# Kernel tuning notes

Hardware: AMD Instinct MI355X
Metric: run time of the kernel (lower is better)

## Reference

```python
import jax, jax.numpy as jnp
import numpy as np
from jax import lax

DN = ('NCHW', 'OIHW', 'NCHW')

def conv2d(x, w, b):
    y = lax.conv_general_dilated(x, w, (1, 1), 'SAME', dimension_numbers=DN)
    return y + b[None, :, None, None]


def setup_inputs() -> dict:
    key = jax.random.key(0)
    ks = jax.random.split(key, 12)
    B, H, W = 16, 256, 256
    def wt(k, shape):
        return jax.random.normal(k, shape, jnp.float32) * 0.05
    return {
        'x': jax.random.normal(ks[0], (B, 1, H, W), jnp.float32),
        'g': jax.random.normal(ks[1], (B, 1, H, W), jnp.float32),
        # conv1 branch (x): 1->64 relu 64->1
        'w1a': wt(ks[2], (64, 1, 3, 3)), 'b1a': jnp.zeros((64,), jnp.float32),
        'w1b': wt(ks[3], (1, 64, 3, 3)), 'b1b': jnp.zeros((1,), jnp.float32),
        # conv2 branch (g): 1->64 relu 64->1
        'w2a': wt(ks[4], (64, 1, 3, 3)), 'b2a': jnp.zeros((64,), jnp.float32),
        'w2b': wt(ks[5], (1, 64, 3, 3)), 'b2b': jnp.zeros((1,), jnp.float32),
        # dynamic filter head: 2->64 relu 64->64 relu 64->81, softmax over taps
        'wfa': wt(ks[6], (64, 2, 3, 3)), 'bfa': jnp.zeros((64,), jnp.float32),
        'wfb': wt(ks[7], (64, 64, 3, 3)), 'bfb': jnp.zeros((64,), jnp.float32),
        'wfc': wt(ks[8], (81, 64, 3, 3)), 'bfc': jnp.zeros((81,), jnp.float32),
    }


def reference(x, g, w1a, b1a, w1b, b1b, w2a, b2a, w2b, b2b,
              wfa, bfa, wfb, bfb, wfc, bfc):
    # feature branches -> 1 channel each
    x_ = conv2d(jax.nn.relu(conv2d(x, w1a, b1a)), w1b, b1b)   # [B,1,H,W]
    g_ = conv2d(jax.nn.relu(conv2d(g, w2a, b2a)), w2b, b2b)   # [B,1,H,W]
    feat = jnp.concatenate([x_, g_], axis=1)                   # [B,2,H,W]
    # per-pixel 9x9 dynamic filter (81 taps), softmax-normalized
    h = jax.nn.relu(conv2d(feat, wfa, bfa))
    h = jax.nn.relu(conv2d(h, wfb, bfb))
    filt = jax.nn.softmax(conv2d(h, wfc, bfc), axis=1)         # [B,81,H,W]
    # unfold: 9x9 neighborhoods with zero pad 4, row-major tap order
    # matches torch unfold(2,9,1).unfold(3,9,1).permute(0,1,4,5,2,3)
    patches = lax.conv_general_dilated_patches(
        x, (9, 9), (1, 1), padding=((4, 4), (4, 4)),
        dimension_numbers=DN)                                  # [B,81,H,W]
    out = jnp.sum(patches * filt, axis=1, keepdims=True)       # [B,1,H,W]
    return out
```

## Files before the change

### kernel.cpp

```cpp
#include <hip/hip_runtime.h>

#define NB 16
#define HH 256
#define WW 256
#define NPIX (HH*WW)

typedef _Float16 f16;
typedef _Float16 f16x8 __attribute__((ext_vector_type(8)));
typedef float f32x4 __attribute__((ext_vector_type(4)));

__device__ __forceinline__ int swzoff(int p, int c) {
    return p * 64 + ((((c >> 3) ^ (p & 7)) << 3) | (c & 7));
}

__global__ __launch_bounds__(256) void prepack_kernel(
    const float* __restrict__ w1a, const float* __restrict__ w2a,
    const float* __restrict__ w1b, const float* __restrict__ w2b,
    const float* __restrict__ wfa, const float* __restrict__ wfb,
    const float* __restrict__ wfc,
    f16* __restrict__ pA1, f16* __restrict__ pA2, f16* __restrict__ pWa,
    f16* __restrict__ pBs1, f16* __restrict__ pBs2,
    f16* __restrict__ pWbF, f16* __restrict__ pWcF)
{
    int i = blockIdx.x * 256 + threadIdx.x;
    if (i < 2048) {
        int c = i >> 5, k = i & 31;
        pA1[i] = (f16)(k < 9 ? w1a[c * 9 + k] : 0.f);
        pA2[i] = (f16)(k < 9 ? w2a[c * 9 + k] : 0.f);
        pWa[i] = (f16)(k < 18 ? wfa[c * 18 + k] : 0.f);
    }
    if (i < 1024) {
        int r = i >> 6, cin = i & 63;
        pBs1[i] = (f16)(r < 9 ? w1b[cin * 9 + r] : 0.f);
        pBs2[i] = (f16)(r < 9 ? w2b[cin * 9 + r] : 0.f);
    }
    if (i < 36864) {
        int kk = i / 2048, r = i & 2047;
        int mt = r >> 9, e = r & 511;
        int l = e >> 3, j = e & 7;
        int cout = mt * 16 + (l & 15);
        int k = kk * 32 + ((l >> 4) << 3) + j;
        int tap = k >> 6, cin = k & 63;
        pWbF[i] = (f16)wfb[(cout * 64 + cin) * 9 + tap];
    }
    if (i < 55296) {
        int kk = i / 3072, r = i % 3072;
        int mt = r >> 9, e = r & 511;
        int l = e >> 3, j = e & 7;
        int cout = mt * 16 + (l & 15);
        int k = kk * 32 + ((l >> 4) << 3) + j;
        int tap = k >> 6, cin = k & 63;
        pWcF[i] = (f16)(cout < 81 ? wfc[(cout * 64 + cin) * 9 + tap] : 0.f);
    }
}

__global__ __launch_bounds__(256, 3) void k1_branch(
    const float* __restrict__ x, const float* __restrict__ g,
    const float* __restrict__ b1a, const float* __restrict__ b2a,
    const float* __restrict__ b1b, const float* __restrict__ b2b,
    const f16* __restrict__ pA1, const f16* __restrict__ pA2,
    const f16* __restrict__ pBs1, const f16* __restrict__ pBs2,
    float* __restrict__ feat)
{
    __shared__ f16 xt[400];
    __shared__ f16 hid[20736];
    __shared__ f16 part[9 * 328];
    __shared__ float bA[64];

    const int tid = threadIdx.x;
    const int wid = tid >> 6, lane = tid & 63;
    const int gq = lane >> 4, cl = lane & 15;
    const int x0 = blockIdx.x * 16, y0 = blockIdx.y * 16;
    const int b = blockIdx.z >> 1, br = blockIdx.z & 1;

    const float* in = (br ? g : x) + (size_t)b * NPIX;
    const f16* pA = br ? pA2 : pA1;
    const f16* pBs = br ? pBs2 : pBs1;
    const float bscal = (br ? b2b : b1b)[0];

    for (int t = tid; t < 400; t += 256) {
        int r = t / 20, c = t % 20;
        int gy = y0 - 2 + r, gx = x0 - 2 + c;
        xt[t] = (f16)(((unsigned)gy < (unsigned)HH && (unsigned)gx < (unsigned)WW)
                          ? in[gy * WW + gx] : 0.f);
    }
    if (tid < 64) bA[tid] = (br ? b2a : b1a)[tid];

    int koff[8];
    #pragma unroll
    for (int j = 0; j < 8; j++) {
        int k = gq * 8 + j;
        int kc = k < 9 ? k : 0;
        koff[j] = (kc / 3) * 20 + (kc % 3);
    }

    f16x8 afA[4];
    #pragma unroll
    for (int mt = 0; mt < 4; mt++)
        afA[mt] = *(const f16x8*)&pA[(mt * 16 + cl) * 32 + gq * 8];
    f16x8 afS0 = *(const f16x8*)&pBs[cl * 64 + gq * 8];
    f16x8 afS1 = *(const f16x8*)&pBs[cl * 64 + 32 + gq * 8];
    __syncthreads();

    #pragma unroll
    for (int it = 0; it < 6; it++) {
        int nt = wid + it * 4;
        if (nt < 21) {
            int p = nt * 16 + cl;
            int pc = p > 323 ? 323 : p;
            int py = pc / 18, px = pc - 18 * py;
            int base = py * 20 + px;
            f16x8 bf;
            #pragma unroll
            for (int j = 0; j < 8; j++) bf[j] = xt[base + koff[j]];
            int gy = y0 - 1 + py, gx = x0 - 1 + px;
            bool ok = (p < 324) &&
                      ((unsigned)gy < (unsigned)HH && (unsigned)gx < (unsigned)WW);
            #pragma unroll
            for (int mt = 0; mt < 4; mt++) {
                f32x4 z = {0.f, 0.f, 0.f, 0.f};
                f32x4 acc = __builtin_amdgcn_mfma_f32_16x16x32_f16(afA[mt], bf, z, 0, 0, 0);
                if (p < 324) {
                    int c0 = mt * 16 + gq * 4;
                    union { f16 h[4]; uint2 u2; } pk;
                    #pragma unroll
                    for (int r = 0; r < 4; r++)
                        pk.h[r] = (f16)(ok ? fmaxf(acc[r] + bA[c0 + r], 0.f) : 0.f);
                    *(uint2*)&hid[swzoff(p, c0)] = pk.u2;
                }
            }
        }
    }
    __syncthreads();

    #pragma unroll
    for (int it = 0; it < 6; it++) {
        int nt = wid + it * 4;
        if (nt < 21) {
            int p = nt * 16 + cl;
            int pc = p > 323 ? 323 : p;
            f16x8 bf0 = *(const f16x8*)&hid[swzoff(pc, gq * 8)];
            f16x8 bf1 = *(const f16x8*)&hid[swzoff(pc, 32 + gq * 8)];
            f32x4 z = {0.f, 0.f, 0.f, 0.f};
            f32x4 d = __builtin_amdgcn_mfma_f32_16x16x32_f16(afS0, bf0, z, 0, 0, 0);
            d = __builtin_amdgcn_mfma_f32_16x16x32_f16(afS1, bf1, d, 0, 0, 0);
            #pragma unroll
            for (int r = 0; r < 4; r++) {
                int tap = gq * 4 + r;
                if (tap < 9 && p < 324)
                    part[tap * 328 + p] = (f16)d[r];
            }
        }
    }
    __syncthreads();

    {
        int ty = tid >> 4, tx = tid & 15;
        float s = bscal;
        #pragma unroll
        for (int u = 0; u < 3; u++)
            #pragma unroll
            for (int v = 0; v < 3; v++)
                s += (float)part[(u * 3 + v) * 328 + (ty + u) * 18 + tx + v];
        feat[((size_t)(b * 2 + br)) * NPIX + (y0 + ty) * WW + x0 + tx] = s;
    }
}

__global__ __launch_bounds__(256, 3) void k2_wfab(
    const float* __restrict__ feat, const f16* __restrict__ pWa,
    const f16* __restrict__ pWbF, const float* __restrict__ bfa,
    const float* __restrict__ bfb, f16* __restrict__ h2g, int b0)
{
    __shared__ f16 ftt[800];
    __shared__ f16 hid[20736];
    __shared__ float bA[64];
    __shared__ float bB[64];

    const int tid = threadIdx.x;
    const int wid = tid >> 6, lane = tid & 63;
    const int gq = lane >> 4, cl = lane & 15;
    const int x0 = blockIdx.x * 16, y0 = blockIdx.y * 16;
    const int ci = blockIdx.z, b = b0 + ci;

    for (int t = tid; t < 800; t += 256) {
        int cin = t / 400, p = t - 400 * cin;
        int r = p / 20, c = p - 20 * r;
        int gy = y0 - 2 + r, gx = x0 - 2 + c;
        ftt[t] = (f16)(((unsigned)gy < (unsigned)HH && (unsigned)gx < (unsigned)WW)
                           ? feat[((size_t)(b * 2 + cin)) * NPIX + gy * WW + gx] : 0.f);
    }
    if (tid < 64) { bA[tid] = bfa[tid]; bB[tid] = bfb[tid]; }

    int koff[8];
    #pragma unroll
    for (int j = 0; j < 8; j++) {
        int k = gq * 8 + j;
        int kc = k < 18 ? k : 0;
        int cin = kc >= 9 ? 1 : 0;
        int tap = kc - 9 * cin;
        koff[j] = cin * 400 + (tap / 3) * 20 + (tap % 3);
    }

    f16x8 afW[4];
    #pragma unroll
    for (int mt = 0; mt < 4; mt++)
        afW[mt] = *(const f16x8*)&pWa[(mt * 16 + cl) * 32 + gq * 8];
    __syncthreads();

    #pragma unroll
    for (int it = 0; it < 6; it++) {
        int nt = wid + it * 4;
        if (nt < 21) {
            int p = nt * 16 + cl;
            int pc = p > 323 ? 323 : p;
            int py = pc / 18, px = pc - 18 * py;
            int base = py * 20 + px;
            f16x8 bf;
            #pragma unroll
            for (int j = 0; j < 8; j++) bf[j] = ftt[base + koff[j]];
            int gy = y0 - 1 + py, gx = x0 - 1 + px;
            bool ok = (p < 324) &&
                      ((unsigned)gy < (unsigned)HH && (unsigned)gx < (unsigned)WW);
            #pragma unroll
            for (int mt = 0; mt < 4; mt++) {
                f32x4 z = {0.f, 0.f, 0.f, 0.f};
                f32x4 acc = __builtin_amdgcn_mfma_f32_16x16x32_f16(afW[mt], bf, z, 0, 0, 0);
                if (p < 324) {
                    int c0 = mt * 16 + gq * 4;
                    union { f16 h[4]; uint2 u2; } pk;
                    #pragma unroll
                    for (int r = 0; r < 4; r++)
                        pk.h[r] = (f16)(ok ? fmaxf(acc[r] + bA[c0 + r], 0.f) : 0.f);
                    *(uint2*)&hid[swzoff(p, c0)] = pk.u2;
                }
            }
        }
    }
    __syncthreads();

    f32x4 acc[4][4];
    #pragma unroll
    for (int i = 0; i < 4; i++)
        #pragma unroll
        for (int mt = 0; mt < 4; mt++) acc[i][mt] = (f32x4){0.f, 0.f, 0.f, 0.f};

    const f16* wfp = pWbF + (size_t)lane * 8;
    f16x8 afA[4], afB[4];
    #pragma unroll
    for (int mt = 0; mt < 4; mt++)
        afA[mt] = *(const f16x8*)&wfp[mt * 512];

    #pragma unroll 1
    for (int kt = 0; kt < 9; kt++) {
        int u = kt / 3, v = kt - 3 * u;
        #pragma unroll
        for (int mt = 0; mt < 4; mt++)
            afB[mt] = *(const f16x8*)&wfp[((2 * kt + 1) * 4 + mt) * 512];
        #pragma unroll
        for (int i = 0; i < 4; i++) {
            int nt = wid * 4 + i;
            int hp = (nt + u) * 18 + cl + v;
            f16x8 bf = *(const f16x8*)&hid[swzoff(hp, gq * 8)];
            #pragma unroll
            for (int mt = 0; mt < 4; mt++)
                acc[i][mt] = __builtin_amdgcn_mfma_f32_16x16x32_f16(afA[mt], bf, acc[i][mt], 0, 0, 0);
        }
        if (kt < 8) {
            #pragma unroll
            for (int mt = 0; mt < 4; mt++)
                afA[mt] = *(const f16x8*)&wfp[((2 * kt + 2) * 4 + mt) * 512];
        }
        #pragma unroll
        for (int i = 0; i < 4; i++) {
            int nt = wid * 4 + i;
            int hp = (nt + u) * 18 + cl + v;
            f16x8 bf = *(const f16x8*)&hid[swzoff(hp, 32 + gq * 8)];
            #pragma unroll
            for (int mt = 0; mt < 4; mt++)
                acc[i][mt] = __builtin_amdgcn_mfma_f32_16x16x32_f16(afB[mt], bf, acc[i][mt], 0, 0, 0);
        }
    }
    #pragma unroll
    for (int i = 0; i < 4; i++) {
        int nt = wid * 4 + i;
        size_t pb = ((size_t)ci * NPIX + (size_t)((y0 + nt) * WW + x0 + cl)) * 64;
        #pragma unroll
        for (int mt = 0; mt < 4; mt++) {
            int c0 = mt * 16 + gq * 4;
            union { f16 h[4]; uint2 u2; } pk;
            #pragma unroll
            for (int r = 0; r < 4; r++)
                pk.h[r] = (f16)fmaxf(acc[i][mt][r] + bB[c0 + r], 0.f);
            *(uint2*)&h2g[pb + c0] = pk.u2;
        }
    }
}

__global__ __launch_bounds__(256, 3) void k3_wfc_apply(
    const f16* __restrict__ h2g, const f16* __restrict__ pWcF,
    const float* __restrict__ bfc, const float* __restrict__ x,
    float* __restrict__ out, int b0)
{
    __shared__ f16 h2t[20736];
    __shared__ float xt24[576];
    __shared__ float bC[96];

    const int tid = threadIdx.x;
    const int wid = tid >> 6, lane = tid & 63;
    const int gq = lane >> 4, cl = lane & 15;
    const int x0 = blockIdx.x * 16, y0 = blockIdx.y * 16;
    const int ci = blockIdx.z, b = b0 + ci;

    for (int t = tid; t < 2592; t += 256) {
        int p = t >> 3, grp = t & 7;
        int py = p / 18, px = p - 18 * py;
        int gy = y0 - 1 + py, gx = x0 - 1 + px;
        f16x8 v = {};
        if ((unsigned)gy < (unsigned)HH && (unsigned)gx < (unsigned)WW)
            v = *(const f16x8*)&h2g[((size_t)ci * NPIX + (size_t)(gy * WW + gx)) * 64 + grp * 8];
        *(f16x8*)&h2t[swzoff(p, grp * 8)] = v;
    }
    const float* xb = x + (size_t)b * NPIX;
    for (int t = tid; t < 576; t += 256) {
        int r = t / 24, c = t - 24 * r;
        int gy = y0 - 4 + r, gx = x0 - 4 + c;
        xt24[t] = ((unsigned)gy < (unsigned)HH && (unsigned)gx < (unsigned)WW)
                      ? xb[gy * WW + gx] : 0.f;
    }
    if (tid < 96) bC[tid] = tid < 81 ? bfc[tid] : 0.f;
    __syncthreads();

    f32x4 acc[4][6];
    #pragma unroll
    for (int i = 0; i < 4; i++)
        #pragma unroll
        for (int mt = 0; mt < 6; mt++) acc[i][mt] = (f32x4){0.f, 0.f, 0.f, 0.f};

    const f16* wfp = pWcF + (size_t)lane * 8;
    f16x8 afA[6], afB[6];
    #pragma unroll
    for (int mt = 0; mt < 6; mt++)
        afA[mt] = *(const f16x8*)&wfp[mt * 512];

    #pragma unroll 1
    for (int kt = 0; kt < 9; kt++) {
        int u = kt / 3, v = kt - 3 * u;
        #pragma unroll
        for (int mt = 0; mt < 6; mt++)
            afB[mt] = *(const f16x8*)&wfp[((2 * kt + 1) * 6 + mt) * 512];
        #pragma unroll
        for (int i = 0; i < 4; i++) {
            int nt = wid * 4 + i;
            int hp = (nt + u) * 18 + cl + v;
            f16x8 bf = *(const f16x8*)&h2t[swzoff(hp, gq * 8)];
            #pragma unroll
            for (int mt = 0; mt < 6; mt++)
                acc[i][mt] = __builtin_amdgcn_mfma_f32_16x16x32_f16(afA[mt], bf, acc[i][mt], 0, 0, 0);
        }
        if (kt < 8) {
            #pragma unroll
            for (int mt = 0; mt < 6; mt++)
                afA[mt] = *(const f16x8*)&wfp[((2 * kt + 2) * 6 + mt) * 512];
        }
        #pragma unroll
        for (int i = 0; i < 4; i++) {
            int nt = wid * 4 + i;
            int hp = (nt + u) * 18 + cl + v;
            f16x8 bf = *(const f16x8*)&h2t[swzoff(hp, 32 + gq * 8)];
            #pragma unroll
            for (int mt = 0; mt < 6; mt++)
                acc[i][mt] = __builtin_amdgcn_mfma_f32_16x16x32_f16(afB[mt], bf, acc[i][mt], 0, 0, 0);
        }
    }

    #pragma unroll
    for (int i = 0; i < 4; i++) {
        int nt = wid * 4 + i;
        float val[6][4];
        float m = -1e30f;
        #pragma unroll
        for (int mt = 0; mt < 6; mt++)
            #pragma unroll
            for (int r = 0; r < 4; r++) {
                int c = mt * 16 + gq * 4 + r;
                float vv = (c <= 80) ? acc[i][mt][r] + bC[c] : -1e30f;
                val[mt][r] = vv;
                m = fmaxf(m, vv);
            }
        m = fmaxf(m, __shfl_xor(m, 16));
        m = fmaxf(m, __shfl_xor(m, 32));
        float s = 0.f, o = 0.f;
        #pragma unroll
        for (int mt = 0; mt < 6; mt++)
            #pragma unroll
            for (int r = 0; r < 4; r++) {
                int c = mt * 16 + gq * 4 + r;
                if (c <= 80) {
                    float e = __expf(val[mt][r] - m);
                    int u9 = c / 9, v9 = c - 9 * u9;
                    s += e;
                    o += e * xt24[(nt + u9) * 24 + cl + v9];
                }
            }
        s += __shfl_xor(s, 16); s += __shfl_xor(s, 32);
        o += __shfl_xor(o, 16); o += __shfl_xor(o, 32);
        if (gq == 0)
            out[(size_t)b * NPIX + (y0 + nt) * WW + x0 + cl] = o / s;
    }
}

extern "C" void kernel_launch(void* const* d_in, const int* in_sizes, int n_in,
                              void* d_out, int out_size, void* d_ws, size_t ws_size,
                              hipStream_t stream)
{
    const float* x   = (const float*)d_in[0];
    const float* g   = (const float*)d_in[1];
    const float* w1a = (const float*)d_in[2];  const float* b1a = (const float*)d_in[3];
    const float* w1b = (const float*)d_in[4];  const float* b1b = (const float*)d_in[5];
    const float* w2a = (const float*)d_in[6];  const float* b2a = (const float*)d_in[7];
    const float* w2b = (const float*)d_in[8];  const float* b2b = (const float*)d_in[9];
    const float* wfa = (const float*)d_in[10]; const float* bfa = (const float*)d_in[11];
    const float* wfb = (const float*)d_in[12]; const float* bfb = (const float*)d_in[13];
    const float* wfc = (const float*)d_in[14]; const float* bfc = (const float*)d_in[15];
    float* out = (float*)d_out;

    float* feat = (float*)d_ws;
    size_t featB = 2097152ull * 4;
    size_t pkB = 100352ull * 2;
    int nbc = 16;
    while (nbc > 1 && featB + (size_t)nbc * NPIX * 64 * 2 + pkB > ws_size) nbc >>= 1;

    f16* h2g = (f16*)((char*)d_ws + featB);
    f16* pk  = h2g + (size_t)nbc * NPIX * 64;
    f16* pA1  = pk;
    f16* pA2  = pA1 + 2048;
    f16* pWa  = pA2 + 2048;
    f16* pBs1 = pWa + 2048;
    f16* pBs2 = pBs1 + 1024;
    f16* pWbF = pBs2 + 1024;
    f16* pWcF = pWbF + 36864;

    prepack_kernel<<<dim3(216), 256, 0, stream>>>(
        w1a, w2a, w1b, w2b, wfa, wfb, wfc, pA1, pA2, pWa, pBs1, pBs2, pWbF, pWcF);

    k1_branch<<<dim3(16, 16, 32), 256, 0, stream>>>(
        x, g, b1a, b2a, b1b, b2b, pA1, pA2, pBs1, pBs2, feat);

    for (int b0 = 0; b0 < NB; b0 += nbc) {
        int cn = (NB - b0) < nbc ? (NB - b0) : nbc;
        k2_wfab<<<dim3(16, 16, cn), 256, 0, stream>>>(
            feat, pWa, pWbF, bfa, bfb, h2g, b0);
        k3_wfc_apply<<<dim3(16, 16, cn), 256, 0, stream>>>(
            h2g, pWcF, bfc, x, out, b0);
    }
}
```

Before: 321.9 us.

## Switch wfc conv in k3 to 32x32x16 MFMA with repacked weights

Replaces the 16x16x32 MFMA tiling of the 64->81 wfc conv in k3 with 32x32x16 MFMAs, covering 96 output channels in 3 groups of 32 and pixel tiles of two 16-wide rows. The wfc weights are repacked in prepack to match the new fragment layout. The fused softmax/apply epilogue is remapped to the new accumulator layout, masking padded channels through the bias (-1e30) and padding the x tile. s_setprio is also raised around the MFMA bursts. The intent is fewer LDS B-fragment reads and fewer MFMA issues per FLOP, at the cost of a different register footprint and a more complex epilogue index mapping.

```diff
diff --git a/kernel.cpp b/kernel.cpp
--- a/kernel.cpp
+++ b/kernel.cpp
@@ -8,6 +8,7 @@
 typedef _Float16 f16;
 typedef _Float16 f16x8 __attribute__((ext_vector_type(8)));
 typedef float f32x4 __attribute__((ext_vector_type(4)));
+typedef float f32x16 __attribute__((ext_vector_type(16)));
 
 __device__ __forceinline__ int swzoff(int p, int c) {
     return p * 64 + ((((c >> 3) ^ (p & 7)) << 3) | (c & 7));
@@ -20,7 +21,7 @@
     const float* __restrict__ wfc,
     f16* __restrict__ pA1, f16* __restrict__ pA2, f16* __restrict__ pWa,
     f16* __restrict__ pBs1, f16* __restrict__ pBs2,
-    f16* __restrict__ pWbF, f16* __restrict__ pWcF)
+    f16* __restrict__ pWbF, f16* __restrict__ pWcG)
 {
     int i = blockIdx.x * 256 + threadIdx.x;
     if (i < 2048) {
@@ -44,13 +45,13 @@
         pWbF[i] = (f16)wfb[(cout * 64 + cin) * 9 + tap];
     }
     if (i < 55296) {
-        int kk = i / 3072, r = i % 3072;
-        int mt = r >> 9, e = r & 511;
+        int q = i / 1536, r = i % 1536;
+        int grp = r >> 9, e = r & 511;
         int l = e >> 3, j = e & 7;
-        int cout = mt * 16 + (l & 15);
-        int k = kk * 32 + ((l >> 4) << 3) + j;
+        int cout = grp * 32 + (l & 31);
+        int k = q * 16 + ((l >> 5) << 3) + j;
         int tap = k >> 6, cin = k & 63;
-        pWcF[i] = (f16)(cout < 81 ? wfc[(cout * 64 + cin) * 9 + tap] : 0.f);
+        pWcG[i] = (f16)(cout < 81 ? wfc[(cout * 64 + cin) * 9 + tap] : 0.f);
     }
 }
 
@@ -297,17 +298,19 @@
 }
 
 __global__ __launch_bounds__(256, 3) void k3_wfc_apply(
-    const f16* __restrict__ h2g, const f16* __restrict__ pWcF,
+    const f16* __restrict__ h2g, const f16* __restrict__ pWcG,
     const float* __restrict__ bfc, const float* __restrict__ x,
     float* __restrict__ out, int b0)
 {
     __shared__ f16 h2t[20736];
-    __shared__ float xt24[576];
+    __shared__ float xt24[648];
     __shared__ float bC[96];
 
     const int tid = threadIdx.x;
     const int wid = tid >> 6, lane = tid & 63;
-    const int gq = lane >> 4, cl = lane & 15;
+    const int col = lane & 31, hi = lane >> 5;
+    const int r10 = col >> 4, cc = col & 15;
+    const int hi8 = hi << 3;
     const int x0 = blockIdx.x * 16, y0 = blockIdx.y * 16;
     const int ci = blockIdx.z, b = b0 + ci;
 
@@ -321,91 +324,98 @@
         *(f16x8*)&h2t[swzoff(p, grp * 8)] = v;
     }
     const float* xb = x + (size_t)b * NPIX;
-    for (int t = tid; t < 576; t += 256) {
-        int r = t / 24, c = t - 24 * r;
-        int gy = y0 - 4 + r, gx = x0 - 4 + c;
-        xt24[t] = ((unsigned)gy < (unsigned)HH && (unsigned)gx < (unsigned)WW)
-                      ? xb[gy * WW + gx] : 0.f;
-    }
-    if (tid < 96) bC[tid] = tid < 81 ? bfc[tid] : 0.f;
-    __syncthreads();
-
-    f32x4 acc[4][6];
-    #pragma unroll
-    for (int i = 0; i < 4; i++)
-        #pragma unroll
-        for (int mt = 0; mt < 6; mt++) acc[i][mt] = (f32x4){0.f, 0.f, 0.f, 0.f};
-
-    const f16* wfp = pWcF + (size_t)lane * 8;
-    f16x8 afA[6], afB[6];
-    #pragma unroll
-    for (int mt = 0; mt < 6; mt++)
-        afA[mt] = *(const f16x8*)&wfp[mt * 512];
+    for (int t = tid; t < 648; t += 256) {
+        float v = 0.f;
+        if (t < 576) {
+            int r = t / 24, c = t - 24 * r;
+            int gy = y0 - 4 + r, gx = x0 - 4 + c;
+            if ((unsigned)gy < (unsigned)HH && (unsigned)gx < (unsigned)WW)
+                v = xb[gy * WW + gx];
+        }
+        xt24[t] = v;
+    }
+    if (tid < 96) bC[tid] = tid < 81 ? bfc[tid] : -1e30f;
+    __syncthreads();
+
+    f32x16 acc[2][3];
+    #pragma unroll
+    for (int gi = 0; gi < 2; gi++)
+        #pragma unroll
+        for (int grp = 0; grp < 3; grp++)
+            acc[gi][grp] = (f32x16){0.f, 0.f, 0.f, 0.f, 0.f, 0.f, 0.f, 0.f,
+                                    0.f, 0.f, 0.f, 0.f, 0.f, 0.f, 0.f, 0.f};
+
+    const f16* wfp = pWcG + (size_t)lane * 8;
+    f16x8 afA[3], afB[3];
+    #pragma unroll
+    for (int grp = 0; grp < 3; grp++)
+        afA[grp] = *(const f16x8*)&wfp[grp * 512];
+
+#define K3_STEP(QV, AF)                                                     \
+    {                                                                       \
+        int tap_ = (QV) >> 2;                                               \
+        int u_ = tap_ / 3, v_ = tap_ - 3 * u_;                              \
+        int cin_ = (((QV) & 3) << 4) + hi8;                                 \
+        _Pragma("unroll")                                                   \
+        for (int gi = 0; gi < 2; gi++) {                                    \
+            int hp_ = (2 * (wid + 4 * gi) + r10 + u_) * 18 + cc + v_;       \
+            f16x8 bf_ = *(const f16x8*)&h2t[swzoff(hp_, cin_)];             \
+            __builtin_amdgcn_s_setprio(1);                                  \
+            _Pragma("unroll")                                               \
+            for (int grp = 0; grp < 3; grp++)                               \
+                acc[gi][grp] = __builtin_amdgcn_mfma_f32_32x32x16_f16(      \
+                    AF[grp], bf_, acc[gi][grp], 0, 0, 0);                   \
+            __builtin_amdgcn_s_setprio(0);                                  \
+        }                                                                   \
+    }
 
     #pragma unroll 1
-    for (int kt = 0; kt < 9; kt++) {
-        int u = kt / 3, v = kt - 3 * u;
-        #pragma unroll
-        for (int mt = 0; mt < 6; mt++)
-            afB[mt] = *(const f16x8*)&wfp[((2 * kt + 1) * 6 + mt) * 512];
-        #pragma unroll
-        for (int i = 0; i < 4; i++) {
-            int nt = wid * 4 + i;
-            int hp = (nt + u) * 18 + cl + v;
-            f16x8 bf = *(const f16x8*)&h2t[swzoff(hp, gq * 8)];
-            #pragma unroll
-            for (int mt = 0; mt < 6; mt++)
-                acc[i][mt] = __builtin_amdgcn_mfma_f32_16x16x32_f16(afA[mt], bf, acc[i][mt], 0, 0, 0);
-        }
-        if (kt < 8) {
-            #pragma unroll
-            for (int mt = 0; mt < 6; mt++)
-                afA[mt] = *(const f16x8*)&wfp[((2 * kt + 2) * 6 + mt) * 512];
-        }
-        #pragma unroll
-        for (int i = 0; i < 4; i++) {
-            int nt = wid * 4 + i;
-            int hp = (nt + u) * 18 + cl + v;
-            f16x8 bf = *(const f16x8*)&h2t[swzoff(hp, 32 + gq * 8)];
-            #pragma unroll
-            for (int mt = 0; mt < 6; mt++)
-                acc[i][mt] = __builtin_amdgcn_mfma_f32_16x16x32_f16(afB[mt], bf, acc[i][mt], 0, 0, 0);
-        }
-    }
-
-    #pragma unroll
-    for (int i = 0; i < 4; i++) {
-        int nt = wid * 4 + i;
-        float val[6][4];
+    for (int qt = 0; qt < 18; qt++) {
+        int q0 = 2 * qt, q1 = 2 * qt + 1;
+        #pragma unroll
+        for (int grp = 0; grp < 3; grp++)
+            afB[grp] = *(const f16x8*)&wfp[(q1 * 3 + grp) * 512];
+        K3_STEP(q0, afA);
+        if (qt < 17) {
+            #pragma unroll
+            for (int grp = 0; grp < 3; grp++)
+                afA[grp] = *(const f16x8*)&wfp[((q1 + 1) * 3 + grp) * 512];
+        }
+        K3_STEP(q1, afB);
+    }
+#undef K3_STEP
+
+    #pragma unroll
+    for (int gi = 0; gi < 2; gi++) {
+        int nt = 2 * (wid + 4 * gi) + r10;
         float m = -1e30f;
         #pragma unroll
-        for (int mt = 0; mt < 6; mt++)
-            #pragma unroll
-            for (int r = 0; r < 4; r++) {
-                int c = mt * 16 + gq * 4 + r;
-                float vv = (c <= 80) ? acc[i][mt][r] + bC[c] : -1e30f;
-                val[mt][r] = vv;
+        for (int grp = 0; grp < 3; grp++)
+            #pragma unroll
+            for (int reg = 0; reg < 16; reg++) {
+                int cbase = grp * 32 + (reg & 3) + 8 * (reg >> 2);
+                float vv = acc[gi][grp][reg] + bC[cbase + 4 * hi];
+                acc[gi][grp][reg] = vv;
                 m = fmaxf(m, vv);
             }
-        m = fmaxf(m, __shfl_xor(m, 16));
         m = fmaxf(m, __shfl_xor(m, 32));
         float s = 0.f, o = 0.f;
         #pragma unroll
-        for (int mt = 0; mt < 6; mt++)
-            #pragma unroll
-            for (int r = 0; r < 4; r++) {
-                int c = mt * 16 + gq * 4 + r;
-                if (c <= 80) {
-                    float e = __expf(val[mt][r] - m);
-                    int u9 = c / 9, v9 = c - 9 * u9;
-                    s += e;
-                    o += e * xt24[(nt + u9) * 24 + cl + v9];
-                }
+        for (int grp = 0; grp < 3; grp++)
+            #pragma unroll
+            for (int reg = 0; reg < 16; reg++) {
+                int cbase = grp * 32 + (reg & 3) + 8 * (reg >> 2);
+                int xo0 = (cbase / 9) * 24 + (cbase % 9);
+                int xo1 = ((cbase + 4) / 9) * 24 + ((cbase + 4) % 9);
+                int xoff = hi ? xo1 : xo0;
+                float e = __expf(acc[gi][grp][reg] - m);
+                s += e;
+                o += e * xt24[nt * 24 + cc + xoff];
             }
-        s += __shfl_xor(s, 16); s += __shfl_xor(s, 32);
-        o += __shfl_xor(o, 16); o += __shfl_xor(o, 32);
-        if (gq == 0)
-            out[(size_t)b * NPIX + (y0 + nt) * WW + x0 + cl] = o / s;
+        s += __shfl_xor(s, 32);
+        o += __shfl_xor(o, 32);
+        if (hi == 0)
+            out[(size_t)b * NPIX + (y0 + nt) * WW + x0 + cc] = o / s;
     }
 }
 
@@ -438,10 +448,10 @@
     f16* pBs1 = pWa + 2048;
     f16* pBs2 = pBs1 + 1024;
     f16* pWbF = pBs2 + 1024;
-    f16* pWcF = pWbF + 36864;
+    f16* pWcG = pWbF + 36864;
 
     prepack_kernel<<<dim3(216), 256, 0, stream>>>(
-        w1a, w2a, w1b, w2b, wfa, wfb, wfc, pA1, pA2, pWa, pBs1, pBs2, pWbF, pWcF);
+        w1a, w2a, w1b, w2b, wfa, wfb, wfc, pA1, pA2, pWa, pBs1, pBs2, pWbF, pWcG);
 
     k1_branch<<<dim3(16, 16, 32), 256, 0, stream>>>(
         x, g, b1a, b2a, b1b, b2b, pA1, pA2, pBs1, pBs2, feat);
@@ -451,6 +461,6 @@
         k2_wfab<<<dim3(16, 16, cn), 256, 0, stream>>>(
             feat, pWa, pWbF, bfa, bfb, h2g, b0);
         k3_wfc_apply<<<dim3(16, 16, cn), 256, 0, stream>>>(
-            h2g, pWcF, bfc, x, out, b0);
-    }
-}
+            h2g, pWcG, bfc, x, out, b0);
+    }
+}
```

Measured after the change: 333.4 us. +3.6%, slower.
